# Kernel tuning notes

Hardware: AMD Instinct MI355X
Metric: run time of the kernel (lower is better)

The kernel has to match this reference:

```python
import jax, jax.numpy as jnp
import numpy as np

K_MASK = -2.3819763e+38

B, T, D = 2, 2048, 2048
N_HEADS, N_KV, HEAD_DIM = 16, 8, 128
SCALAR = 0.08838834764831845  # head_dim ** -0.5
ROPE_BASE = 10000


def rms_norm(x, scale):
    # fp32 mean-of-squares, rsqrt, bf16 round-trip, then scale (as in QwemmaRMSNorm)
    x32 = x.astype(jnp.float32)
    var = jnp.mean(jnp.square(x32), axis=-1, keepdims=True)
    rescaled = (x32 * jax.lax.rsqrt(var + 1e-06)).astype(jnp.bfloat16)
    return rescaled * scale


def apply_rope(inputs, positions, base_frequency):
    head_dim = inputs.shape[-1]
    fraction = 2 * jnp.arange(0, head_dim // 2) / head_dim
    timescale = base_frequency ** fraction
    sinusoid = positions[..., jnp.newaxis] / timescale[jnp.newaxis, jnp.newaxis, :]
    sinusoid = sinusoid[..., jnp.newaxis, :]  # [B,T,1,H/2]
    sin = jnp.sin(sinusoid).astype(inputs.dtype)
    cos = jnp.cos(sinusoid).astype(inputs.dtype)
    first, second = jnp.split(inputs, 2, axis=-1)
    out = jnp.concatenate([first * cos - second * sin,
                           second * cos + first * sin], axis=-1)
    return out.astype(inputs.dtype)


def setup_inputs() -> dict:
    key = jax.random.key(0)
    ks = jax.random.split(key, 7)
    x = jax.random.normal(ks[0], (B, T, D), dtype=jnp.float32)
    segment_pos = jnp.broadcast_to(jnp.arange(T, dtype=jnp.int32)[None, :], (B, T))
    attn_mask = jnp.broadcast_to(jnp.tril(jnp.ones((T, T), dtype=bool))[None], (B, T, T))
    q_w = jax.random.normal(ks[1], (N_HEADS, D, HEAD_DIM), dtype=jnp.float32) * 0.02
    kv_w = jax.random.normal(ks[2], (2, N_KV, D, HEAD_DIM), dtype=jnp.float32) * 0.02
    o_w = jax.random.normal(ks[3], (N_HEADS, HEAD_DIM, D), dtype=jnp.float32) * 0.02
    q_scale = 1.0 + 0.1 * jax.random.normal(ks[4], (HEAD_DIM,), dtype=jnp.float32)
    k_scale = 1.0 + 0.1 * jax.random.normal(ks[5], (HEAD_DIM,), dtype=jnp.float32)
    return {"x": x, "segment_pos": segment_pos, "attn_mask": attn_mask,
            "q_w": q_w, "kv_w": kv_w, "o_w": o_w,
            "q_scale": q_scale, "k_scale": k_scale}


def reference(x, segment_pos, attn_mask, q_w, kv_w, o_w, q_scale, k_scale):
    # projections
    q = jnp.einsum('BTD,NDH->BTNH', x, q_w)
    k, v = jnp.einsum('BSD,CKDH->CBSKH', x, kv_w)
    # QK RMSNorm + RoPE
    q = apply_rope(rms_norm(q, q_scale), segment_pos, ROPE_BASE)
    k = apply_rope(rms_norm(k, k_scale), segment_pos, ROPE_BASE)
    # GQA: [B,T,N,H] -> [B,T,K,G,H]
    b, t, n, h = q.shape
    g = n // N_KV
    q = q.reshape((b, t, N_KV, g, h))
    logits = jnp.einsum('BTKGH,BSKH->BTKGS', q, k)
    logits = (logits.astype(jnp.float32) * SCALAR).astype(jnp.bfloat16)
    s = logits.shape[-1]
    logits = logits.reshape((b, t, n, s))
    padded = jnp.where(jnp.expand_dims(attn_mask, -2), logits, K_MASK)
    probs = jax.nn.softmax(padded.astype(jnp.float32), axis=-1).astype(k.dtype)
    probs = probs.reshape((b, t, N_KV, g, s))
    encoded = jnp.einsum('BTKGS,BSKH->BTKGH', probs, v)
    encoded = encoded.reshape((b, t, n, h))
    return jnp.einsum('BTNH,NHD->BTD', encoded, o_w)


if __name__ == '__main__':
    out = reference(**setup_inputs())
    print(out.shape, out.dtype)
```

## Files before the change

kernel.cpp:

```cpp
#include <hip/hip_runtime.h>

typedef unsigned short u16;
typedef __attribute__((ext_vector_type(4))) float f32x4;
typedef __attribute__((ext_vector_type(8))) short s16x8;

#define SCALAR_F 0.08838834764831845f
#define KMASKF (-1e30f)

__device__ __forceinline__ u16 f2b(float f){
  unsigned u = __float_as_uint(f);
  unsigned r = u + 0x7FFFu + ((u>>16)&1u);
  return (u16)(r>>16);
}
__device__ __forceinline__ float b2f(u16 h){ return __uint_as_float(((unsigned)h)<<16); }

__device__ __forceinline__ f32x4 mfma16(s16x8 a, s16x8 b, f32x4 c){
  return __builtin_amdgcn_mfma_f32_16x16x32_bf16(a, b, c, 0, 0, 0);
}

__device__ __forceinline__ void glds16(const u16* g, u16* l){
  __builtin_amdgcn_global_load_lds((const __attribute__((address_space(1))) unsigned*)g,
                                   (__attribute__((address_space(3))) unsigned*)l, 16, 0, 0);
}

__global__ __launch_bounds__(256) void cvt_f32_bf16(const float* __restrict__ in, u16* __restrict__ out){
  int i = blockIdx.x*256 + threadIdx.x;
  const float4* p = (const float4*)in;
  float4 a = p[2*i], b = p[2*i+1];
  s16x8 r;
  r[0]=(short)f2b(a.x); r[1]=(short)f2b(a.y); r[2]=(short)f2b(a.z); r[3]=(short)f2b(a.w);
  r[4]=(short)f2b(b.x); r[5]=(short)f2b(b.y); r[6]=(short)f2b(b.z); r[7]=(short)f2b(b.w);
  *(s16x8*)(out + (size_t)i*8) = r;
}

__global__ __launch_bounds__(256) void build_wqkvt(const float* __restrict__ qw, const float* __restrict__ kvw,
                                                   u16* __restrict__ out){
  __shared__ float t[64][65];
  int head = blockIdx.z;
  int d0 = blockIdx.y*64, h0 = blockIdx.x*64;
  const float* src; int colbase;
  if (head < 16){ src = qw + (size_t)head*2048*128; colbase = head*128; }
  else if (head < 24){ int k = head-16; src = kvw + (size_t)k*2048*128; colbase = 2048 + k*128; }
  else { int k = head-24; src = kvw + (size_t)(8+k)*2048*128; colbase = 3072 + k*128; }
  int tid = threadIdx.x;
  #pragma unroll
  for (int p=0;p<16;p++){ int e = p*256+tid; int r = e>>6, c = e&63;
    t[r][c] = src[(size_t)(d0+r)*128 + h0 + c]; }
  __syncthreads();
  #pragma unroll
  for (int p=0;p<16;p++){ int e = p*256+tid; int c = e>>6, r = e&63;
    out[(size_t)(colbase + h0 + c)*2048 + d0 + r] = f2b(t[r][c]); }
}

__global__ __launch_bounds__(256) void tr2048(const float* __restrict__ src, u16* __restrict__ out){
  __shared__ float t[64][65];
  int r0 = blockIdx.y*64, c0 = blockIdx.x*64;
  int tid = threadIdx.x;
  #pragma unroll
  for (int p=0;p<16;p++){ int e = p*256+tid; int r = e>>6, c = e&63;
    t[r][c] = src[(size_t)(r0+r)*2048 + c0 + c]; }
  __syncthreads();
  #pragma unroll
  for (int p=0;p<16;p++){ int e = p*256+tid; int c = e>>6, r = e&63;
    out[(size_t)(c0+c)*2048 + r0 + r] = f2b(t[r][c]); }
}

__global__ __launch_bounds__(256) void rope_table(float* __restrict__ table){
  int tid = blockIdx.x*256 + threadIdx.x;
  int pos = tid>>6, i = tid&63;
  float ts = powf(10000.f, (float)i * (1.f/64.f));
  float ang = (float)pos / ts;
  ((float2*)table)[tid] = make_float2(sinf(ang), cosf(ang));
}

template<bool OUTBF16>
__global__ __launch_bounds__(256) void gemm_bt(const u16* __restrict__ A, const u16* __restrict__ Bt,
                                               void* __restrict__ C, int K, int ldc){
  __shared__ u16 As[128*64];
  __shared__ u16 Bs[128*64];
  const int tid = threadIdx.x, w = tid>>6, l = tid&63;
  const int wm = w>>1, wn = w&1;
  const int l15 = l&15, lg = l>>4, l7 = l&7;
  const size_t m0 = (size_t)blockIdx.y*128, n0 = (size_t)blockIdx.x*128;
  const f32x4 z4 = {0.f,0.f,0.f,0.f};
  f32x4 acc[4][4];
  #pragma unroll
  for (int m=0;m<4;m++)
    #pragma unroll
    for (int n=0;n<4;n++) acc[m][n] = z4;
  const char* AsB = (const char*)As; const char* BsB = (const char*)Bs;
  int colsw[2];
  colsw[0] = (lg*16) ^ (l7<<4);
  colsw[1] = (64 + lg*16) ^ (l7<<4);
  int arow[4], brow[4];
  #pragma unroll
  for (int m=0;m<4;m++){ arow[m] = (wm*64 + m*16 + l15)*128; brow[m] = (wn*64 + m*16 + l15)*128; }
  const int sgl = l7 ^ (l>>3);
  for (int k0=0;k0<K;k0+=64){
    #pragma unroll
    for (int i=0;i<4;i++){
      int slot = (w*4+i)*64 + l;
      int row = slot>>3;
      glds16(A  + (m0+row)*K + k0 + sgl*8, (u16*)As + slot*8);
      glds16(Bt + (n0+row)*K + k0 + sgl*8, (u16*)Bs + slot*8);
    }
    __syncthreads();
    #pragma unroll
    for (int kb=0;kb<2;kb++){
      s16x8 af[4], bf[4];
      #pragma unroll
      for (int m=0;m<4;m++) af[m] = *(const s16x8*)(AsB + arow[m] + colsw[kb]);
      #pragma unroll
      for (int n=0;n<4;n++) bf[n] = *(const s16x8*)(BsB + brow[n] + colsw[kb]);
      #pragma unroll
      for (int m=0;m<4;m++)
        #pragma unroll
        for (int n=0;n<4;n++)
          acc[m][n] = mfma16(af[m], bf[n], acc[m][n]);
    }
    __syncthreads();
  }
  #pragma unroll
  for (int m=0;m<4;m++)
    #pragma unroll
    for (int n=0;n<4;n++)
      #pragma unroll
      for (int r=0;r<4;r++){
        size_t row = m0 + wm*64 + m*16 + lg*4 + r;
        size_t col = n0 + wn*64 + n*16 + l15;
        if (OUTBF16) ((u16*)C)[row*ldc + col] = f2b(acc[m][n][r]);
        else ((float*)C)[row*ldc + col] = acc[m][n][r];
      }
}

__global__ __launch_bounds__(256) void norm_rope(const u16* __restrict__ qkv, const float* __restrict__ table,
                                                 const float* __restrict__ scale, const int* __restrict__ segpos,
                                                 u16* __restrict__ dst, int nhl2, int colbase, float mult){
  int w = threadIdx.x>>6, l = threadIdx.x&63;
  int rid = blockIdx.x*4 + w;
  int bt = rid >> nhl2;
  int n  = rid & ((1<<nhl2)-1);
  int b = bt >> 11, t = bt & 2047;
  const u16* src = qkv + (size_t)bt*4096 + colbase + n*128;
  float x1 = b2f(src[l]), x2 = b2f(src[64+l]);
  float ss = x1*x1 + x2*x2;
  #pragma unroll
  for (int off=32; off; off>>=1) ss += __shfl_xor(ss, off);
  float rs = rsqrtf(ss*(1.f/128.f) + 1e-6f);
  float v1 = x1*rs*scale[l], v2 = x2*rs*scale[64+l];
  int pos = segpos[bt];
  float2 sc = ((const float2*)table)[pos*64 + l];
  float o1 = (v1*sc.y - v2*sc.x)*mult;
  float o2 = (v2*sc.y + v1*sc.x)*mult;
  u16* d = dst + (((size_t)((b<<nhl2) + n))*2048 + t)*128;
  d[l] = f2b(o1); d[64+l] = f2b(o2);
}

__global__ __launch_bounds__(256) void vtr(const u16* __restrict__ qkv, u16* __restrict__ vt){
  __shared__ float t[64][65];
  int bk = blockIdx.z;
  int t0 = blockIdx.y*64, d0 = blockIdx.x*64;
  int b = bk>>3, kv = bk&7;
  int tid = threadIdx.x;
  #pragma unroll
  for (int p=0;p<16;p++){ int e = p*256+tid; int r = e>>6, c = e&63;
    t[r][c] = b2f(qkv[(size_t)(b*2048 + t0 + r)*4096 + 3072 + kv*128 + d0 + c]); }
  __syncthreads();
  #pragma unroll
  for (int p=0;p<16;p++){ int e = p*256+tid; int c = e>>6, r = e&63;
    vt[((size_t)bk*128 + d0 + c)*2048 + t0 + r] = f2b(t[r][c]); }
}

__global__ __launch_bounds__(256,2) void attn_kern(const u16* __restrict__ qn, const u16* __restrict__ kn,
                                                   const u16* __restrict__ vt, u16* __restrict__ enc){
  __shared__ u16 Ks[2][64*128];
  __shared__ u16 Vs[2][64*128];
  __shared__ u16 Ps[4*16*64];
  const int idx = blockIdx.x;
  const int pp = idx>>5;
  const int hb = idx & 31;
  const int hn = hb & 15, b = hb >> 4;
  const int kv = hn>>1;
  const int tid = threadIdx.x, w = tid>>6, l = tid&63;
  const int l15 = l&15, lg = l>>4;
  const u16* qh = qn + ((size_t)(b*16+hn))*2048*128;
  const u16* kh = kn + ((size_t)(b*8+kv))*2048*128;
  const u16* vh = vt + ((size_t)(b*8+kv))*128*2048;
  const int qbA = pp, qbB = 31-pp;

  int qr0 = qbA*64 + w*16;
  s16x8 qf[4];
  #pragma unroll
  for (int kb=0;kb<4;kb++)
    qf[kb] = *(const s16x8*)(qh + (size_t)(qr0 + l15)*128 + kb*32 + lg*8);

  const f32x4 z4 = {0.f,0.f,0.f,0.f};
  f32x4 o[8];
  #pragma unroll
  for (int dn=0;dn<8;dn++) o[dn] = z4;
  float mrow[4], lp[4];
  #pragma unroll
  for (int r=0;r<4;r++){ mrow[r] = KMASKF; lp[r] = 0.f; }

  const char* KsB0 = (const char*)&Ks[0][0];
  const char* VsB0 = (const char*)&Vs[0][0];
  char* PsB = (char*)Ps + w*2048;

  auto stage = [&](int s0, int bi){
    #pragma unroll
    for (int i=0;i<4;i++){
      int slot = (w*4+i)*64 + l;
      { int row = slot>>4, g = slot&15, gl = g ^ (row&7);
        glds16(kh + (size_t)(s0+row)*128 + gl*8, &Ks[bi][0] + slot*8); }
      { int row = slot>>3, g = slot&7, gl = g ^ (row&7);
        glds16(vh + (size_t)row*2048 + s0 + gl*8, &Vs[bi][0] + slot*8); }
    }
  };

  auto epilogue = [&](int qr){
    #pragma unroll
    for (int r=0;r<4;r++){
      float s = lp[r];
      s += __shfl_xor(s,1); s += __shfl_xor(s,2); s += __shfl_xor(s,4); s += __shfl_xor(s,8);
      lp[r] = 1.f/s;
    }
    #pragma unroll
    for (int dn=0;dn<8;dn++)
      #pragma unroll
      for (int r=0;r<4;r++){
        size_t row = (size_t)b*2048 + qr + lg*4 + r;
        size_t col = hn*128 + dn*16 + l15;
        enc[row*2048 + col] = f2b(o[dn][r]*lp[r]);
      }
  };

  stage(0, 0);
  __syncthreads();

  int cur = 0;
  for (int it=0; it<=32; ++it){
    if (it < 32){
      int s0n = (it+1 <= pp) ? (it+1)*64 : (it-pp)*64;
      stage(s0n, cur^1);
    }
    const int s0 = (it <= pp) ? it*64 : (it-pp-1)*64;
    const char* KsB = KsB0 + cur*16384;
    const char* VsB = VsB0 + cur*16384;

    f32x4 sa[4];
    #pragma unroll
    for (int nc=0;nc<4;nc++) sa[nc] = z4;
    #pragma unroll
    for (int kb=0;kb<4;kb++){
      s16x8 kf[4];
      #pragma unroll
      for (int nc=0;nc<4;nc++){
        int srow = nc*16 + l15;
        int cb = (kb*64 + lg*16) ^ ((srow&7)<<4);
        kf[nc] = *(const s16x8*)(KsB + srow*256 + cb);
      }
      #pragma unroll
      for (int nc=0;nc<4;nc++)
        sa[nc] = mfma16(qf[kb], kf[nc], sa[nc]);
    }
    if (it == pp || it == 32){
      #pragma unroll
      for (int nc=0;nc<4;nc++)
        #pragma unroll
        for (int r=0;r<4;r++){
          int row = qr0 + lg*4 + r;
          int col = s0 + nc*16 + l15;
          if (col > row) sa[nc][r] = KMASKF;
        }
    }
    #pragma unroll
    for (int r=0;r<4;r++){
      float pm = fmaxf(fmaxf(sa[0][r], sa[1][r]), fmaxf(sa[2][r], sa[3][r]));
      pm = fmaxf(pm, __shfl_xor(pm,1));
      pm = fmaxf(pm, __shfl_xor(pm,2));
      pm = fmaxf(pm, __shfl_xor(pm,4));
      pm = fmaxf(pm, __shfl_xor(pm,8));
      float mo = mrow[r];
      float mn = fmaxf(mo, pm);
      float sc = __expf(mo - mn);
      mrow[r] = mn;
      int rowp = lg*4 + r;
      float ls = 0.f;
      #pragma unroll
      for (int nc=0;nc<4;nc++){
        float p = __expf(sa[nc][r] - mn);
        ls += p;
        int cb = ((nc*16 + l15)*2) ^ ((rowp&7)<<4);
        *(u16*)(PsB + rowp*128 + cb) = f2b(p);
      }
      lp[r] = lp[r]*sc + ls;
      #pragma unroll
      for (int dn=0;dn<8;dn++) o[dn][r] *= sc;
    }
    asm volatile("" ::: "memory");
    #pragma unroll
    for (int kb=0;kb<2;kb++){
      int rowp = l15;
      int cbp = (kb*64 + lg*16) ^ ((rowp&7)<<4);
      s16x8 pf = *(const s16x8*)(PsB + rowp*128 + cbp);
      #pragma unroll
      for (int dn=0;dn<8;dn++){
        int vrow = dn*16 + l15;
        int cb = (kb*64 + lg*16) ^ ((vrow&7)<<4);
        s16x8 vf = *(const s16x8*)(VsB + vrow*128 + cb);
        o[dn] = mfma16(pf, vf, o[dn]);
      }
    }
    if (it == pp){
      epilogue(qr0);
      qr0 = qbB*64 + w*16;
      #pragma unroll
      for (int kb=0;kb<4;kb++)
        qf[kb] = *(const s16x8*)(qh + (size_t)(qr0 + l15)*128 + kb*32 + lg*8);
      #pragma unroll
      for (int dn=0;dn<8;dn++) o[dn] = z4;
      #pragma unroll
      for (int r=0;r<4;r++){ mrow[r] = KMASKF; lp[r] = 0.f; }
    }
    __syncthreads();
    cur ^= 1;
  }
  epilogue(qr0);
}

extern "C" void kernel_launch(void* const* d_in, const int* in_sizes, int n_in,
                              void* d_out, int out_size, void* d_ws, size_t ws_size,
                              hipStream_t stream){
  const float* x      = (const float*)d_in[0];
  const int*   segpos = (const int*)d_in[1];
  const float* qw     = (const float*)d_in[3];
  const float* kvw    = (const float*)d_in[4];
  const float* ow     = (const float*)d_in[5];
  const float* qs     = (const float*)d_in[6];
  const float* ks     = (const float*)d_in[7];
  float* out = (float*)d_out;

  char* ws = (char*)d_ws;
  size_t off = 0;
  auto alloc = [&](size_t bytes)->void*{ void* p = ws + off; off += (bytes + 255) & ~(size_t)255; return p; };
  u16*   xb    = (u16*)alloc((size_t)4096*2048*2);
  u16*   wqkvt = (u16*)alloc((size_t)4096*2048*2);
  u16*   wot   = (u16*)alloc((size_t)2048*2048*2);
  u16*   qkv   = (u16*)alloc((size_t)4096*4096*2);
  u16*   qn    = (u16*)alloc((size_t)2*16*2048*128*2);
  u16*   kn    = (u16*)alloc((size_t)2*8*2048*128*2);
  u16*   vt    = (u16*)alloc((size_t)2*8*128*2048*2);
  u16*   enc   = (u16*)alloc((size_t)4096*2048*2);
  float* table = (float*)alloc((size_t)2048*64*2*4);

  cvt_f32_bf16<<<4096,256,0,stream>>>(x, xb);
  build_wqkvt<<<dim3(2,32,32),256,0,stream>>>(qw, kvw, wqkvt);
  tr2048<<<dim3(32,32),256,0,stream>>>(ow, wot);
  rope_table<<<512,256,0,stream>>>(table);
  gemm_bt<true><<<dim3(32,32),256,0,stream>>>(xb, wqkvt, qkv, 2048, 4096);
  norm_rope<<<16384,256,0,stream>>>(qkv, table, qs, segpos, qn, 4, 0,    SCALAR_F);
  norm_rope<<<8192, 256,0,stream>>>(qkv, table, ks, segpos, kn, 3, 2048, 1.0f);
  vtr<<<dim3(2,32,16),256,0,stream>>>(qkv, vt);
  attn_kern<<<512,256,0,stream>>>(qn, kn, vt, enc);
  gemm_bt<false><<<dim3(16,32),256,0,stream>>>(enc, wot, out, 2048, 2048);
}
```

Measured before the change: 384.7 us.

## Replace QKV projection GEMM with 256x256-tile, 4-stage pipelined LDS kernel

```diff
diff --git a/kernel.cpp b/kernel.cpp
--- a/kernel.cpp
+++ b/kernel.cpp
@@ -71,6 +71,83 @@
   float ts = powf(10000.f, (float)i * (1.f/64.f));
   float ang = (float)pos / ts;
   ((float2*)table)[tid] = make_float2(sinf(ang), cosf(ang));
+}
+
+__global__ __launch_bounds__(512,2) void gemm256(const u16* __restrict__ A, const u16* __restrict__ Bt,
+                                                 u16* __restrict__ C, int K, int ldc){
+  __shared__ u16 Asw[4][256*32];
+  __shared__ u16 Bsw[4][256*32];
+  const int tid = threadIdx.x;
+  const int wid = tid>>6, l = tid&63;
+  const int wr = wid>>2, wc = wid&3;
+  const int l15 = l&15, lg = l>>4;
+  const int wg = blockIdx.x;
+  const int swz = (wg&7)*32 + (wg>>3);
+  const size_t m0 = (size_t)(swz>>4)*256, n0 = (size_t)(swz&15)*256;
+
+  const f32x4 z4 = {0.f,0.f,0.f,0.f};
+  f32x4 acc[8][4];
+  #pragma unroll
+  for (int mi=0;mi<8;mi++)
+    #pragma unroll
+    for (int ni=0;ni<4;ni++) acc[mi][ni] = z4;
+
+  auto stage = [&](int k0, int bi){
+    #pragma unroll
+    for (int c=0;c<2;c++){
+      int g = c*512 + tid;
+      int row = g>>2;
+      int sc = (g&3) ^ ((g>>3)&3);
+      glds16(A  + (m0+row)*K + k0 + sc*8, &Asw[bi][0] + g*8);
+      glds16(Bt + (n0+row)*K + k0 + sc*8, &Bsw[bi][0] + g*8);
+    }
+  };
+
+  auto compute = [&](int bi){
+    const char* AsB = (const char*)&Asw[bi][0];
+    const char* BsB = (const char*)&Bsw[bi][0];
+    s16x8 bfr[4];
+    #pragma unroll
+    for (int ni=0;ni<4;ni++){
+      int r = wc*64 + ni*16 + l15;
+      bfr[ni] = *(const s16x8*)(BsB + r*64 + ((lg*16) ^ (((r>>1)&3)<<4)));
+    }
+    __builtin_amdgcn_s_setprio(1);
+    #pragma unroll
+    for (int mi=0;mi<8;mi++){
+      int r = wr*128 + mi*16 + l15;
+      s16x8 af = *(const s16x8*)(AsB + r*64 + ((lg*16) ^ (((r>>1)&3)<<4)));
+      #pragma unroll
+      for (int ni=0;ni<4;ni++)
+        acc[mi][ni] = mfma16(af, bfr[ni], acc[mi][ni]);
+    }
+    __builtin_amdgcn_s_setprio(0);
+  };
+
+  const int NT = K>>5;
+  stage(0,0); stage(32,1); stage(64,2);
+  asm volatile("s_waitcnt vmcnt(8)" ::: "memory");
+  __builtin_amdgcn_s_barrier();
+  for (int t=0; t<NT; ++t){
+    if (t+3 < NT) stage((t+3)<<5, (t+3)&3);
+    compute(t&3);
+    int rem = NT-1-t;
+    if (rem >= 3)      { asm volatile("s_waitcnt vmcnt(8)" ::: "memory"); }
+    else if (rem == 2) { asm volatile("s_waitcnt vmcnt(4)" ::: "memory"); }
+    else if (rem == 1) { asm volatile("s_waitcnt vmcnt(0)" ::: "memory"); }
+    __builtin_amdgcn_s_barrier();
+  }
+
+  #pragma unroll
+  for (int mi=0;mi<8;mi++)
+    #pragma unroll
+    for (int ni=0;ni<4;ni++)
+      #pragma unroll
+      for (int r=0;r<4;r++){
+        size_t row = m0 + wr*128 + mi*16 + lg*4 + r;
+        size_t col = n0 + wc*64 + ni*16 + l15;
+        C[row*ldc + col] = f2b(acc[mi][ni][r]);
+      }
 }
 
 template<bool OUTBF16>
@@ -357,7 +434,7 @@
   build_wqkvt<<<dim3(2,32,32),256,0,stream>>>(qw, kvw, wqkvt);
   tr2048<<<dim3(32,32),256,0,stream>>>(ow, wot);
   rope_table<<<512,256,0,stream>>>(table);
-  gemm_bt<true><<<dim3(32,32),256,0,stream>>>(xb, wqkvt, qkv, 2048, 4096);
+  gemm256<<<256,512,0,stream>>>(xb, wqkvt, qkv, 2048, 4096);
   norm_rope<<<16384,256,0,stream>>>(qkv, table, qs, segpos, qn, 4, 0,    SCALAR_F);
   norm_rope<<<8192, 256,0,stream>>>(qkv, table, ks, segpos, kn, 3, 2048, 1.0f);
   vtr<<<dim3(2,32,16),256,0,stream>>>(qkv, vt);
```

New measurement: 380.6 us. About the same (-1.1%).
